# Kernel tuning notes

Hardware: AMD Instinct MI355X
Metric: run time of the kernel (lower is better)

The kernel has to match this reference:

```python
import jax, jax.numpy as jnp
import numpy as np

NA = 50000
NB = 50000
E = 800000
D = 256


def setup_inputs() -> dict:
    key = jax.random.key(0)
    ks = jax.random.split(key, 7)
    feature_a = jax.random.normal(ks[0], (NA, D), dtype=jnp.float32)
    feature_b = jax.random.normal(ks[1], (NB, D), dtype=jnp.float32)
    # Linear(b_dim, b_dim): store weight pre-transposed so new_emb = feature_b @ W + b
    W = jax.random.normal(ks[2], (D, D), dtype=jnp.float32) * (1.0 / np.sqrt(D))
    b = jnp.zeros((D,), dtype=jnp.float32)
    # kaiming-normal-ish init for attention vector a: [a_dim + b_dim, 1]
    a = jax.random.normal(ks[3], (2 * D, 1), dtype=jnp.float32) * np.sqrt(2.0 / (2 * D))
    edge_src = jnp.sort(jax.random.randint(ks[4], (E,), 0, NA, dtype=jnp.int32)).astype(jnp.int64)
    edge_dst = jax.random.randint(ks[5], (E,), 0, NB, dtype=jnp.int64)
    return {
        "feature_a": feature_a,
        "feature_b": feature_b,
        "W": W,
        "b": b,
        "a": a,
        "edge_src": edge_src,
        "edge_dst": edge_dst,
        "node_num_a": NA,
        "node_num_b": NB,
    }


def reference(feature_a, feature_b, W, b, a, edge_src, edge_dst, node_num_a, node_num_b):
    # new_emb = out_mlp_layer(feature_b)
    new_emb = feature_b @ W + b  # [Nb, D]

    # cat([feature_a[src], new_emb[dst]]) @ a  ==  (feature_a @ a_top)[src] + (new_emb @ a_bot)[dst]
    a_dim = feature_a.shape[1]
    a_top = a[:a_dim, 0]   # [a_dim]
    a_bot = a[a_dim:, 0]   # [b_dim]
    s_a = feature_a @ a_top   # [Na]
    s_b = new_emb @ a_bot     # [Nb]
    logits = s_a[edge_src] + s_b[edge_dst]  # [E]

    # exp(elu(x, alpha=0.1))
    elu = jnp.where(logits > 0, logits, 0.1 * jnp.expm1(logits))
    score = jnp.exp(elu)  # [E]

    # sparse mm: weighted aggregation of new_emb over edges, grouped by src
    msg = score[:, None] * new_emb[edge_dst]  # [E, D]
    agg = jax.ops.segment_sum(msg, edge_src, num_segments=node_num_a)       # [Na, D]
    row_sum = jax.ops.segment_sum(score, edge_src, num_segments=node_num_a)  # [Na]
    row_sum = jnp.where(row_sum == 0, 1.0, row_sum)[:, None]
    return agg / row_sum
```

## Files before the change

kernel.cpp:

```cpp
#include <hip/hip_runtime.h>
#include <cstdint>

#define NA_N 50000
#define NB_N 50000
#define NE_N 800000
#define DD 256

using bf8   = __attribute__((ext_vector_type(8))) short;
using f32x4 = __attribute__((ext_vector_type(4))) float;
using u16x8 = __attribute__((ext_vector_type(8))) ushort;

__device__ __forceinline__ ushort f2bf(float f) {
    uint u = __float_as_uint(f);
    uint r = (u + 0x7fffu + ((u >> 16) & 1u)) >> 16;
    return (ushort)r;
}
__device__ __forceinline__ float bf2f(ushort u) {
    return __uint_as_float(((uint)u) << 16);
}

__global__ __launch_bounds__(256) void wt_cast(const float* __restrict__ W,
                                               ushort* __restrict__ Wt)
{
    __shared__ float T[64][65];
    const int bi = blockIdx.x & 3;
    const int bj = blockIdx.x >> 2;
    const int lane = threadIdx.x & 63, w = threadIdx.x >> 6;
    for (int i = w; i < 64; i += 4)
        T[i][lane] = W[(size_t)(bi * 64 + i) * DD + bj * 64 + lane];
    __syncthreads();
    for (int i = w; i < 64; i += 4)
        Wt[(size_t)(bj * 64 + i) * DD + bi * 64 + lane] = f2bf(T[lane][i]);
}

__global__ __launch_bounds__(256) void gemm_mfma(
    const float* __restrict__ A, const ushort* __restrict__ Wt,
    const float* __restrict__ bias, const float* __restrict__ a_bot,
    ushort* __restrict__ C, float* __restrict__ s_b)
{
    __shared__ ushort As[64 * 264];
    __shared__ float  sdot[4][64];
    const int t  = threadIdx.x;
    const int r0 = blockIdx.x * 64;

#pragma unroll
    for (int i = 0; i < 16; i++) {
        int flat = i * 256 + t;
        int row  = flat >> 6;
        int c4   = flat & 63;
        int gr   = r0 + row; if (gr >= NB_N) gr = 0;
        float4 v = ((const float4*)(A + (size_t)gr * DD))[c4];
        ushort4 b;
        b.x = f2bf(v.x); b.y = f2bf(v.y); b.z = f2bf(v.z); b.w = f2bf(v.w);
        *(ushort4*)&As[row * 264 + c4 * 4] = b;
    }
    __syncthreads();

    const int lane = t & 63;
    const int wv   = t >> 6;
    const int lr   = lane & 15;
    const int lk   = (lane >> 4) * 8;

    f32x4 acc[4][4];
#pragma unroll
    for (int m = 0; m < 4; m++)
#pragma unroll
        for (int n = 0; n < 4; n++) acc[m][n] = (f32x4){0.f, 0.f, 0.f, 0.f};

#pragma unroll
    for (int ks = 0; ks < 8; ks++) {
        const int k0 = ks * 32;
        bf8 af[4], bb[4];
#pragma unroll
        for (int m = 0; m < 4; m++)
            af[m] = *(const bf8*)&As[(m * 16 + lr) * 264 + k0 + lk];
#pragma unroll
        for (int n = 0; n < 4; n++) {
            int col = wv * 64 + n * 16 + lr;
            bb[n] = *(const bf8*)&Wt[(size_t)col * DD + k0 + lk];
        }
#pragma unroll
        for (int m = 0; m < 4; m++)
#pragma unroll
            for (int n = 0; n < 4; n++)
                acc[m][n] = __builtin_amdgcn_mfma_f32_16x16x32_bf16(
                    af[m], bb[n], acc[m][n], 0, 0, 0);
    }

    float abv[4];
#pragma unroll
    for (int n = 0; n < 4; n++) abv[n] = a_bot[wv * 64 + n * 16 + lr];

    float part[4][4];
#pragma unroll
    for (int m = 0; m < 4; m++)
#pragma unroll
        for (int r = 0; r < 4; r++) part[m][r] = 0.f;

#pragma unroll
    for (int m = 0; m < 4; m++)
#pragma unroll
        for (int n = 0; n < 4; n++) {
            int   col = wv * 64 + n * 16 + lr;
            float bv  = bias[col];
#pragma unroll
            for (int r = 0; r < 4; r++) {
                int   rowg = r0 + m * 16 + (lane >> 4) * 4 + r;
                float v    = acc[m][n][r] + bv;
                if (rowg < NB_N) C[(size_t)rowg * DD + col] = f2bf(v);
                part[m][r] = fmaf(v, abv[n], part[m][r]);
            }
        }

#pragma unroll
    for (int m = 0; m < 4; m++)
#pragma unroll
        for (int r = 0; r < 4; r++) {
#pragma unroll
            for (int off = 1; off < 16; off <<= 1)
                part[m][r] += __shfl_xor(part[m][r], off, 64);
        }
    if (lr == 0) {
#pragma unroll
        for (int m = 0; m < 4; m++)
#pragma unroll
            for (int r = 0; r < 4; r++)
                sdot[wv][m * 16 + (lane >> 4) * 4 + r] = part[m][r];
    }
    __syncthreads();
    if (t < 64) {
        int rowg = r0 + t;
        if (rowg < NB_N)
            s_b[rowg] = sdot[0][t] + sdot[1][t] + sdot[2][t] + sdot[3][t];
    }
}

__global__ __launch_bounds__(256) void rowdot(const float* __restrict__ M,
    const float* __restrict__ v, float* __restrict__ out, int nrows)
{
    const int lane = threadIdx.x & 63;
    const int row  = blockIdx.x * 4 + (threadIdx.x >> 6);
    if (row >= nrows) return;
    float4 av = ((const float4*)(M + (size_t)row * DD))[lane];
    float4 bv = ((const float4*)v)[lane];
    float  s  = av.x * bv.x + av.y * bv.y + av.z * bv.z + av.w * bv.w;
#pragma unroll
    for (int off = 32; off; off >>= 1) s += __shfl_down(s, off, 64);
    if (lane == 0) out[row] = s;
}

__global__ void rowstart_k(const int* __restrict__ esrc, int* __restrict__ row_start)
{
    int e = blockIdx.x * 256 + threadIdx.x;
    if (e >= NE_N) return;
    int s    = esrc[e];
    int prev = (e == 0) ? -1 : esrc[e - 1];
    for (int r = prev + 1; r <= s; r++) row_start[r] = e;
    if (e == NE_N - 1)
        for (int r = s + 1; r <= NA_N; r++) row_start[r] = NE_N;
}

__global__ __launch_bounds__(256) void score_k(
    const int* __restrict__ esrc, const int* __restrict__ edst,
    const float* __restrict__ sa, const float* __restrict__ sb,
    float2* __restrict__ pairs)
{
    int e = blockIdx.x * 256 + threadIdx.x;
    if (e >= NE_N) return;
    int   src = esrc[e], dst = edst[e];
    float lg  = sa[src] + sb[dst];
    float el  = lg > 0.f ? lg : 0.1f * expm1f(lg);
    pairs[e]  = make_float2(expf(el), __int_as_float(dst));
}

__global__ __launch_bounds__(256) void edge_agg3(
    const float2* __restrict__ pairs, const int* __restrict__ row_start,
    const ushort* __restrict__ emb, float* __restrict__ out)
{
    const int lane = threadIdx.x & 63;
    const int a    = blockIdx.x * 4 + (threadIdx.x >> 6);
    if (a >= NA_N) return;

    const int h  = lane >> 5;
    const int c0 = (lane & 31) * 8;
    const int beg = row_start[a], end = row_start[a + 1];

    float acc0 = 0.f, acc1 = 0.f, acc2 = 0.f, acc3 = 0.f;
    float acc4 = 0.f, acc5 = 0.f, acc6 = 0.f, acc7 = 0.f;
    float rs   = 0.f;

    for (int e = beg; e < end; e += 2) {
        const int ee = e + h;
        float s  = 0.f;
        int   dd = 0;
        if (ee < end) {
            float2 pr = pairs[ee];
            s  = pr.x;
            dd = __float_as_int(pr.y);
        }
        u16x8 u = *(const u16x8*)(emb + (size_t)dd * DD + c0);
        acc0 = fmaf(s, bf2f(u[0]), acc0);
        acc1 = fmaf(s, bf2f(u[1]), acc1);
        acc2 = fmaf(s, bf2f(u[2]), acc2);
        acc3 = fmaf(s, bf2f(u[3]), acc3);
        acc4 = fmaf(s, bf2f(u[4]), acc4);
        acc5 = fmaf(s, bf2f(u[5]), acc5);
        acc6 = fmaf(s, bf2f(u[6]), acc6);
        acc7 = fmaf(s, bf2f(u[7]), acc7);
        rs += s;
    }

    acc0 += __shfl_xor(acc0, 32, 64);  acc1 += __shfl_xor(acc1, 32, 64);
    acc2 += __shfl_xor(acc2, 32, 64);  acc3 += __shfl_xor(acc3, 32, 64);
    acc4 += __shfl_xor(acc4, 32, 64);  acc5 += __shfl_xor(acc5, 32, 64);
    acc6 += __shfl_xor(acc6, 32, 64);  acc7 += __shfl_xor(acc7, 32, 64);
    rs   += __shfl_xor(rs, 32, 64);

    const float inv = (rs == 0.f) ? 1.f : (1.f / rs);
    float4 o;
    o.x = (h ? acc4 : acc0) * inv;
    o.y = (h ? acc5 : acc1) * inv;
    o.z = (h ? acc6 : acc2) * inv;
    o.w = (h ? acc7 : acc3) * inv;
    *(float4*)(out + (size_t)a * DD + c0 + h * 4) = o;
}

extern "C" void kernel_launch(void* const* d_in, const int* in_sizes, int n_in,
                              void* d_out, int out_size, void* d_ws, size_t ws_size,
                              hipStream_t stream)
{
    const float* fa   = (const float*)d_in[0];
    const float* fb   = (const float*)d_in[1];
    const float* W    = (const float*)d_in[2];
    const float* bias = (const float*)d_in[3];
    const float* avec = (const float*)d_in[4];
    const int*   esrc = (const int*)d_in[5];
    const int*   edst = (const int*)d_in[6];
    float*       out  = (float*)d_out;

    char*   ws        = (char*)d_ws;
    ushort* emb_b     = (ushort*)ws;
    float2* pairs     = (float2*)(ws + (size_t)NB_N * DD * 2);
    float*  s_a       = (float*)(pairs + NE_N);
    float*  s_b       = s_a + NA_N;
    int*    row_start = (int*)(s_b + NB_N);
    ushort* Wt        = (ushort*)(row_start + NA_N + 2);

    wt_cast  <<<16, 256, 0, stream>>>(W, Wt);
    gemm_mfma<<<(NB_N + 63) / 64, 256, 0, stream>>>(fb, Wt, bias, avec + DD,
                                                    emb_b, s_b);
    rowdot   <<<(NA_N + 3) / 4, 256, 0, stream>>>(fa, avec, s_a, NA_N);
    rowstart_k<<<(NE_N + 255) / 256, 256, 0, stream>>>(esrc, row_start);
    score_k  <<<(NE_N + 255) / 256, 256, 0, stream>>>(esrc, edst, s_a, s_b, pairs);
    edge_agg3<<<(NA_N + 3) / 4, 256, 0, stream>>>(pairs, row_start, emb_b, out);
}
```

Baseline: 126.7 us.

## Fuse row-dot and edge scoring into aggregation kernel, four edges per wave

Drops the separate rowdot and score kernels and the intermediate pairs buffer. The aggregation wave now computes its source row's dot product with a_top, evaluates each edge's score inline from edst and s_b, and processes four edges per iteration with 16 lanes of 16 columns each. This removes two launches and the pairs write and re-read, at the cost of re-reading feature_a inside the aggregation kernel, using fast __expf approximations, and adding more cross-lane reductions at the end.

```diff
diff --git a/kernel.cpp b/kernel.cpp
--- a/kernel.cpp
+++ b/kernel.cpp
@@ -135,20 +135,6 @@
     }
 }
 
-__global__ __launch_bounds__(256) void rowdot(const float* __restrict__ M,
-    const float* __restrict__ v, float* __restrict__ out, int nrows)
-{
-    const int lane = threadIdx.x & 63;
-    const int row  = blockIdx.x * 4 + (threadIdx.x >> 6);
-    if (row >= nrows) return;
-    float4 av = ((const float4*)(M + (size_t)row * DD))[lane];
-    float4 bv = ((const float4*)v)[lane];
-    float  s  = av.x * bv.x + av.y * bv.y + av.z * bv.z + av.w * bv.w;
-#pragma unroll
-    for (int off = 32; off; off >>= 1) s += __shfl_down(s, off, 64);
-    if (lane == 0) out[row] = s;
-}
-
 __global__ void rowstart_k(const int* __restrict__ esrc, int* __restrict__ row_start)
 {
     int e = blockIdx.x * 256 + threadIdx.x;
@@ -160,69 +146,72 @@
         for (int r = s + 1; r <= NA_N; r++) row_start[r] = NE_N;
 }
 
-__global__ __launch_bounds__(256) void score_k(
-    const int* __restrict__ esrc, const int* __restrict__ edst,
-    const float* __restrict__ sa, const float* __restrict__ sb,
-    float2* __restrict__ pairs)
-{
-    int e = blockIdx.x * 256 + threadIdx.x;
-    if (e >= NE_N) return;
-    int   src = esrc[e], dst = edst[e];
-    float lg  = sa[src] + sb[dst];
-    float el  = lg > 0.f ? lg : 0.1f * expm1f(lg);
-    pairs[e]  = make_float2(expf(el), __int_as_float(dst));
-}
-
-__global__ __launch_bounds__(256) void edge_agg3(
-    const float2* __restrict__ pairs, const int* __restrict__ row_start,
-    const ushort* __restrict__ emb, float* __restrict__ out)
+__global__ __launch_bounds__(256) void edge_agg4(
+    const int* __restrict__ edst, const int* __restrict__ row_start,
+    const float* __restrict__ fa, const float* __restrict__ a_top,
+    const float* __restrict__ sb, const ushort* __restrict__ emb,
+    float* __restrict__ out)
 {
     const int lane = threadIdx.x & 63;
     const int a    = blockIdx.x * 4 + (threadIdx.x >> 6);
     if (a >= NA_N) return;
 
-    const int h  = lane >> 5;
-    const int c0 = (lane & 31) * 8;
+    float4 av = ((const float4*)(fa + (size_t)a * DD))[lane];
+    float4 tv = ((const float4*)a_top)[lane];
+    float  sa_a = av.x * tv.x + av.y * tv.y + av.z * tv.z + av.w * tv.w;
+#pragma unroll
+    for (int off = 1; off < 64; off <<= 1) sa_a += __shfl_xor(sa_a, off, 64);
+
+    const int g = lane >> 4;
+    const int c = lane & 15;
     const int beg = row_start[a], end = row_start[a + 1];
 
-    float acc0 = 0.f, acc1 = 0.f, acc2 = 0.f, acc3 = 0.f;
-    float acc4 = 0.f, acc5 = 0.f, acc6 = 0.f, acc7 = 0.f;
-    float rs   = 0.f;
-
-    for (int e = beg; e < end; e += 2) {
-        const int ee = e + h;
-        float s  = 0.f;
-        int   dd = 0;
+    float accA[8], accB[8];
+#pragma unroll
+    for (int j = 0; j < 8; j++) { accA[j] = 0.f; accB[j] = 0.f; }
+    float rs = 0.f;
+
+    for (int e = beg; e < end; e += 4) {
+        const int ee = e + g;
         if (ee < end) {
-            float2 pr = pairs[ee];
-            s  = pr.x;
-            dd = __float_as_int(pr.y);
-        }
-        u16x8 u = *(const u16x8*)(emb + (size_t)dd * DD + c0);
-        acc0 = fmaf(s, bf2f(u[0]), acc0);
-        acc1 = fmaf(s, bf2f(u[1]), acc1);
-        acc2 = fmaf(s, bf2f(u[2]), acc2);
-        acc3 = fmaf(s, bf2f(u[3]), acc3);
-        acc4 = fmaf(s, bf2f(u[4]), acc4);
-        acc5 = fmaf(s, bf2f(u[5]), acc5);
-        acc6 = fmaf(s, bf2f(u[6]), acc6);
-        acc7 = fmaf(s, bf2f(u[7]), acc7);
-        rs += s;
-    }
-
-    acc0 += __shfl_xor(acc0, 32, 64);  acc1 += __shfl_xor(acc1, 32, 64);
-    acc2 += __shfl_xor(acc2, 32, 64);  acc3 += __shfl_xor(acc3, 32, 64);
-    acc4 += __shfl_xor(acc4, 32, 64);  acc5 += __shfl_xor(acc5, 32, 64);
-    acc6 += __shfl_xor(acc6, 32, 64);  acc7 += __shfl_xor(acc7, 32, 64);
-    rs   += __shfl_xor(rs, 32, 64);
-
-    const float inv = (rs == 0.f) ? 1.f : (1.f / rs);
-    float4 o;
-    o.x = (h ? acc4 : acc0) * inv;
-    o.y = (h ? acc5 : acc1) * inv;
-    o.z = (h ? acc6 : acc2) * inv;
-    o.w = (h ? acc7 : acc3) * inv;
-    *(float4*)(out + (size_t)a * DD + c0 + h * 4) = o;
+            int   dd = edst[ee];
+            float lg = sa_a + sb[dd];
+            float el = lg > 0.f ? lg : 0.1f * (__expf(lg) - 1.f);
+            float s  = __expf(el);
+            const ushort* rp = emb + (size_t)dd * DD + c * 16;
+            u16x8 u0 = *(const u16x8*)rp;
+            u16x8 u1 = *(const u16x8*)(rp + 8);
+#pragma unroll
+            for (int j = 0; j < 8; j++) {
+                accA[j] = fmaf(s, bf2f(u0[j]), accA[j]);
+                accB[j] = fmaf(s, bf2f(u1[j]), accB[j]);
+            }
+            rs += s;
+        }
+    }
+
+#pragma unroll
+    for (int j = 0; j < 8; j++) {
+        accA[j] += __shfl_xor(accA[j], 16, 64);
+        accA[j] += __shfl_xor(accA[j], 32, 64);
+        accB[j] += __shfl_xor(accB[j], 16, 64);
+        accB[j] += __shfl_xor(accB[j], 32, 64);
+    }
+    rs += __shfl_xor(rs, 16, 64);
+    rs += __shfl_xor(rs, 32, 64);
+
+    if (g == 0) {
+        const float inv = (rs == 0.f) ? 1.f : (1.f / rs);
+        float* op = out + (size_t)a * DD + c * 16;
+        float4 o0 = { accA[0] * inv, accA[1] * inv, accA[2] * inv, accA[3] * inv };
+        float4 o1 = { accA[4] * inv, accA[5] * inv, accA[6] * inv, accA[7] * inv };
+        float4 o2 = { accB[0] * inv, accB[1] * inv, accB[2] * inv, accB[3] * inv };
+        float4 o3 = { accB[4] * inv, accB[5] * inv, accB[6] * inv, accB[7] * inv };
+        *(float4*)(op + 0)  = o0;
+        *(float4*)(op + 4)  = o1;
+        *(float4*)(op + 8)  = o2;
+        *(float4*)(op + 12) = o3;
+    }
 }
 
 extern "C" void kernel_launch(void* const* d_in, const int* in_sizes, int n_in,
@@ -240,17 +229,14 @@
 
     char*   ws        = (char*)d_ws;
     ushort* emb_b     = (ushort*)ws;
-    float2* pairs     = (float2*)(ws + (size_t)NB_N * DD * 2);
-    float*  s_a       = (float*)(pairs + NE_N);
-    float*  s_b       = s_a + NA_N;
+    float*  s_b       = (float*)(ws + (size_t)NB_N * DD * 2);
     int*    row_start = (int*)(s_b + NB_N);
     ushort* Wt        = (ushort*)(row_start + NA_N + 2);
 
-    wt_cast  <<<16, 256, 0, stream>>>(W, Wt);
-    gemm_mfma<<<(NB_N + 63) / 64, 256, 0, stream>>>(fb, Wt, bias, avec + DD,
-                                                    emb_b, s_b);
-    rowdot   <<<(NA_N + 3) / 4, 256, 0, stream>>>(fa, avec, s_a, NA_N);
+    wt_cast   <<<16, 256, 0, stream>>>(W, Wt);
+    gemm_mfma <<<(NB_N + 63) / 64, 256, 0, stream>>>(fb, Wt, bias, avec + DD,
+                                                     emb_b, s_b);
     rowstart_k<<<(NE_N + 255) / 256, 256, 0, stream>>>(esrc, row_start);
-    score_k  <<<(NE_N + 255) / 256, 256, 0, stream>>>(esrc, edst, s_a, s_b, pairs);
-    edge_agg3<<<(NA_N + 3) / 4, 256, 0, stream>>>(pairs, row_start, emb_b, out);
-}
+    edge_agg4 <<<(NA_N + 3) / 4, 256, 0, stream>>>(edst, row_start, fa, avec,
+                                                   s_b, emb_b, out);
+}
```

Result: faster. 112.3 us (-11.3%).
